# Kernel optimization log

Hardware: AMD Instinct MI355X
Metric: run time of the kernel (lower is better)

Reference implementation:

```python
import jax, jax.numpy as jnp
import numpy as np

B, D, H, O = 16384, 256, 64, 256


def setup_inputs() -> dict:
    key = jax.random.key(0)
    ks = jax.random.split(key, 7)
    s1 = 1.0  # Linear(1,H): fan_in=1 -> U(-1,1)
    sH = 1.0 / np.sqrt(H)
    sD = 1.0 / np.sqrt(D)
    return {
        "x": jax.random.normal(ks[0], (B, D), dtype=jnp.float32),
        "W1": jax.random.uniform(ks[1], (D, H), jnp.float32, -s1, s1),
        "b1": jax.random.uniform(ks[2], (D, H), jnp.float32, -s1, s1),
        "W2": jax.random.uniform(ks[3], (D, H), jnp.float32, -sH, sH),
        "b2": jax.random.uniform(ks[4], (D,), jnp.float32, -sH, sH),
        "Wc": jax.random.uniform(ks[5], (O, D), jnp.float32, -sD, sD),
        "bc": jax.random.uniform(ks[6], (O,), jnp.float32, -sD, sD),
    }


def reference(x, W1, b1, W2, b2, Wc, bc):
    # Per-feature tiny MLP, batched over the feature axis D.
    # hidden: [B, D, H]
    h = jax.nn.relu(x[:, :, None] * W1[None, :, :] + b1[None, :, :])
    # collapse hidden -> scalar per feature: [B, D]
    u = jnp.einsum("bdh,dh->bd", h, W2) + b2[None, :]
    # combiner Linear(D, O)
    return u @ Wc.T + bc[None, :]
```

## Files before the change

kernel.cpp:

```cpp
#include <hip/hip_runtime.h>
#include <hip/hip_fp16.h>

#define B_N 16384
#define D_N 256
#define H_N 64
#define O_N 256

typedef unsigned int u32;
typedef unsigned short u16;
typedef _Float16 f16;
typedef __attribute__((ext_vector_type(2))) _Float16 f16x2;
typedef __attribute__((ext_vector_type(8))) _Float16 f16x8;
typedef __attribute__((ext_vector_type(4))) float f32x4;
typedef __attribute__((ext_vector_type(4))) u32 uint4v;
typedef __attribute__((ext_vector_type(4))) u16 u16x4;

__device__ u32 g_Wp [D_N * 32];
__device__ u32 g_Bp [D_N * 32];
__device__ u32 g_W2p[D_N * 32];
__device__ __attribute__((aligned(16))) u16 g_Wch[O_N * D_N];
__device__ __attribute__((aligned(16))) u16 g_Uf[B_N * D_N];

union HU { f16 h; u16 b; };

static __device__ __forceinline__ u32 packh2(float a, float b) {
  f16x2 p = {(f16)a, (f16)b};
  return __builtin_bit_cast(u32, p);
}
static __device__ __forceinline__ u16 f16b(float a) { HU u; u.h = (f16)a; return u.b; }
static __device__ __forceinline__ f16x2 ash2(u32 w) { return __builtin_bit_cast(f16x2, w); }

#if __has_builtin(__builtin_amdgcn_fdot2)
#define FDOT2(a, b, c) __builtin_amdgcn_fdot2((a), (b), (c), false)
#else
#define FDOT2(a, b, c) \
  fmaf((float)(a)[0], (float)(b)[0], fmaf((float)(a)[1], (float)(b)[1], (c)))
#endif

__global__ __launch_bounds__(256) void prep(
    const float* __restrict__ W1, const float* __restrict__ b1,
    const float* __restrict__ W2, const float* __restrict__ Wc) {
  const int t = blockIdx.x * 256 + threadIdx.x;
  if ((t & 1) == 0) {
    const int d = t >> 6, j = (t & 63) >> 1;
    const int idx = d * 32 + j;
    g_Wp[idx]  = packh2(W1[t], W1[t + 1]);
    g_Bp[idx]  = packh2(b1[t], b1[t + 1]);
    g_W2p[idx] = packh2(W2[t], W2[t + 1]);
  }
  const int i4 = t * 4;
  const f32x4 v = *reinterpret_cast<const f32x4*>(Wc + i4);
  u16x4 s;
#pragma unroll
  for (int q = 0; q < 4; ++q) s[q] = f16b(v[q]);
  *reinterpret_cast<u16x4*>(g_Wch + i4) = s;
}

__global__ __launch_bounds__(256) void kan_p1(const float* __restrict__ x,
                                              const float* __restrict__ b2) {
  const int tid = threadIdx.x;
  const int b   = (blockIdx.x >> 4) * 256 + tid;
  const int d0  = (blockIdx.x & 15) * 16;

  f32x4 xr[4];
#pragma unroll
  for (int c = 0; c < 4; ++c)
    xr[c] = *reinterpret_cast<const f32x4*>(x + b * D_N + d0 + c * 4);

  float uo[16];
#pragma unroll
  for (int c = 0; c < 4; ++c) {
#pragma unroll
    for (int e = 0; e < 4; ++e) {
      const int dd = c * 4 + e;
      const int d  = d0 + dd;
      const f16 hx = (f16)xr[c][e];
      const f16x2 xx = {hx, hx};
      float acc = 0.f;
      const u32* __restrict__ wp  = g_Wp  + d * 32;
      const u32* __restrict__ bp  = g_Bp  + d * 32;
      const u32* __restrict__ w2p = g_W2p + d * 32;
#pragma unroll
      for (int j = 0; j < 32; ++j) {
        f16x2 tv = __builtin_elementwise_fma(xx, ash2(wp[j]), ash2(bp[j]));
        tv = __builtin_elementwise_max(tv, (f16x2){(f16)0.f, (f16)0.f});
        acc = FDOT2(tv, ash2(w2p[j]), acc);
      }
      uo[dd] = acc + b2[d];
    }
  }

  const int base = ((b >> 4) * 32 + (d0 >> 3)) * 128 + (b & 15) * 8;
#pragma unroll
  for (int half = 0; half < 2; ++half) {
    union { u16 h[8]; uint4v v; } pk;
#pragma unroll
    for (int e = 0; e < 8; ++e) pk.h[e] = f16b(uo[half * 8 + e]);
    *reinterpret_cast<uint4v*>(g_Uf + base + half * 128) = pk.v;
  }
}

__global__ __launch_bounds__(256) void kan_p2(const float* __restrict__ bc,
                                              float* __restrict__ out) {
  const int t    = threadIdx.x;
  const int wv   = t >> 6, dl = t & 63;
  const int mt   = blockIdx.x;
  const int n0   = wv * 64;
  const int mrow = dl & 15;
  const int kgrp = dl >> 4;
  const int b0   = mt * 16;

  f32x4 acc2[4];
#pragma unroll
  for (int j = 0; j < 4; ++j) acc2[j] = (f32x4)(0.f);

#pragma unroll
  for (int ks = 0; ks < 8; ++ks) {
    const int k0 = ks * 32 + kgrp * 8;
    const f16x8 afrag = *reinterpret_cast<const f16x8*>(
        g_Uf + (mt * 32 + ks * 4 + kgrp) * 128 + mrow * 8);
#pragma unroll
    for (int j = 0; j < 4; ++j) {
      const f16x8 bfrag = *reinterpret_cast<const f16x8*>(
          g_Wch + (n0 + j * 16 + mrow) * D_N + k0);
      acc2[j] = __builtin_amdgcn_mfma_f32_16x16x32_f16(afrag, bfrag, acc2[j],
                                                       0, 0, 0);
    }
  }

#pragma unroll
  for (int j = 0; j < 4; ++j) {
    const int colg = n0 + j * 16 + mrow;
    const float bcv = bc[colg];
#pragma unroll
    for (int q = 0; q < 4; ++q) {
      const int rowg = b0 + kgrp * 4 + q;
      out[rowg * O_N + colg] = acc2[j][q] + bcv;
    }
  }
}

extern "C" void kernel_launch(void* const* d_in, const int* in_sizes, int n_in,
                              void* d_out, int out_size, void* d_ws, size_t ws_size,
                              hipStream_t stream) {
  const float* x  = (const float*)d_in[0];
  const float* W1 = (const float*)d_in[1];
  const float* b1 = (const float*)d_in[2];
  const float* W2 = (const float*)d_in[3];
  const float* b2 = (const float*)d_in[4];
  const float* Wc = (const float*)d_in[5];
  const float* bc = (const float*)d_in[6];
  float* out = (float*)d_out;

  prep<<<dim3(D_N * H_N / 256), dim3(256), 0, stream>>>(W1, b1, W2, Wc);
  kan_p1<<<dim3((B_N / 256) * (D_N / 16)), dim3(256), 0, stream>>>(x, b2);
  kan_p2<<<dim3(B_N / 16), dim3(256), 0, stream>>>(bc, out);
}
```

Baseline: 118.4 us.

## Stage per-feature weights in LDS via async DMA and reuse across rows

The three packed fp16 weight arrays are interleaved into one buffer, and each wave copies its 8 features' weights into LDS with global_load_lds. In the old code every thread read weights from global memory through scalar loads. Each thread now handles 4 batch rows for 8 features, so every LDS weight vector read is reused across 4 rows. Blocks cover 32 features with a launch bound of 2 waves per SIMD. The tradeoff is higher register pressure from 32 packed x values and a raw vmcnt wait.

```diff
diff --git a/kernel.cpp b/kernel.cpp
--- a/kernel.cpp
+++ b/kernel.cpp
@@ -15,9 +15,7 @@
 typedef __attribute__((ext_vector_type(4))) u32 uint4v;
 typedef __attribute__((ext_vector_type(4))) u16 u16x4;
 
-__device__ u32 g_Wp [D_N * 32];
-__device__ u32 g_Bp [D_N * 32];
-__device__ u32 g_W2p[D_N * 32];
+__device__ __attribute__((aligned(16))) u32 g_Wf[D_N * 96];
 __device__ __attribute__((aligned(16))) u16 g_Wch[O_N * D_N];
 __device__ __attribute__((aligned(16))) u16 g_Uf[B_N * D_N];
 
@@ -37,16 +35,21 @@
   fmaf((float)(a)[0], (float)(b)[0], fmaf((float)(a)[1], (float)(b)[1], (c)))
 #endif
 
+static __device__ __forceinline__ void dma16(const u32* g, u32* l) {
+  __builtin_amdgcn_global_load_lds(
+      (const __attribute__((address_space(1))) u32*)g,
+      (__attribute__((address_space(3))) u32*)l, 16, 0, 0);
+}
+
 __global__ __launch_bounds__(256) void prep(
     const float* __restrict__ W1, const float* __restrict__ b1,
     const float* __restrict__ W2, const float* __restrict__ Wc) {
   const int t = blockIdx.x * 256 + threadIdx.x;
   if ((t & 1) == 0) {
     const int d = t >> 6, j = (t & 63) >> 1;
-    const int idx = d * 32 + j;
-    g_Wp[idx]  = packh2(W1[t], W1[t + 1]);
-    g_Bp[idx]  = packh2(b1[t], b1[t + 1]);
-    g_W2p[idx] = packh2(W2[t], W2[t + 1]);
+    g_Wf[d * 96 + j]      = packh2(W1[t], W1[t + 1]);
+    g_Wf[d * 96 + 32 + j] = packh2(b1[t], b1[t + 1]);
+    g_Wf[d * 96 + 64 + j] = packh2(W2[t], W2[t + 1]);
   }
   const int i4 = t * 4;
   const f32x4 v = *reinterpret_cast<const f32x4*>(Wc + i4);
@@ -56,47 +59,76 @@
   *reinterpret_cast<u16x4*>(g_Wch + i4) = s;
 }
 
-__global__ __launch_bounds__(256) void kan_p1(const float* __restrict__ x,
-                                              const float* __restrict__ b2) {
-  const int tid = threadIdx.x;
-  const int b   = (blockIdx.x >> 4) * 256 + tid;
-  const int d0  = (blockIdx.x & 15) * 16;
+__global__ __launch_bounds__(256, 2) void kan_p1(const float* __restrict__ x,
+                                                 const float* __restrict__ b2) {
+  __shared__ u32 wlds[4 * 768];
 
-  f32x4 xr[4];
+  const int tid  = threadIdx.x;
+  const int lane = tid & 63;
+  const int wv   = tid >> 6;
+  const int bs   = blockIdx.x >> 3;
+  const int dg   = blockIdx.x & 7;
+  const int d0   = dg * 32 + wv * 8;
+  const int rb   = bs * 256 + lane;
+
+  {
+    const u32* src = g_Wf + d0 * 96;
+    u32* dst = wlds + wv * 768;
 #pragma unroll
-  for (int c = 0; c < 4; ++c)
-    xr[c] = *reinterpret_cast<const f32x4*>(x + b * D_N + d0 + c * 4);
+    for (int i = 0; i < 3; ++i) dma16(src + i * 256 + lane * 4, dst + i * 256);
+  }
 
-  float uo[16];
+  f16x2 xx[4][8];
 #pragma unroll
-  for (int c = 0; c < 4; ++c) {
+  for (int r = 0; r < 4; ++r) {
+    const float* xp = x + (size_t)(rb + r * 64) * D_N + d0;
+    const f32x4 a = *reinterpret_cast<const f32x4*>(xp);
+    const f32x4 b = *reinterpret_cast<const f32x4*>(xp + 4);
 #pragma unroll
     for (int e = 0; e < 4; ++e) {
-      const int dd = c * 4 + e;
-      const int d  = d0 + dd;
-      const f16 hx = (f16)xr[c][e];
-      const f16x2 xx = {hx, hx};
-      float acc = 0.f;
-      const u32* __restrict__ wp  = g_Wp  + d * 32;
-      const u32* __restrict__ bp  = g_Bp  + d * 32;
-      const u32* __restrict__ w2p = g_W2p + d * 32;
-#pragma unroll
-      for (int j = 0; j < 32; ++j) {
-        f16x2 tv = __builtin_elementwise_fma(xx, ash2(wp[j]), ash2(bp[j]));
-        tv = __builtin_elementwise_max(tv, (f16x2){(f16)0.f, (f16)0.f});
-        acc = FDOT2(tv, ash2(w2p[j]), acc);
-      }
-      uo[dd] = acc + b2[d];
+      const f16 ha = (f16)a[e], hb = (f16)b[e];
+      xx[r][e]     = (f16x2){ha, ha};
+      xx[r][4 + e] = (f16x2){hb, hb};
     }
   }
 
-  const int base = ((b >> 4) * 32 + (d0 >> 3)) * 128 + (b & 15) * 8;
+  asm volatile("s_waitcnt vmcnt(0)" ::: "memory");
+
+  const u32* wl = wlds + wv * 768;
+  uint4v pkv[4];
 #pragma unroll
-  for (int half = 0; half < 2; ++half) {
-    union { u16 h[8]; uint4v v; } pk;
+  for (int dd = 0; dd < 8; ++dd) {
+    const float b2v = b2[d0 + dd];
+    float acc[4] = {0.f, 0.f, 0.f, 0.f};
 #pragma unroll
-    for (int e = 0; e < 8; ++e) pk.h[e] = f16b(uo[half * 8 + e]);
-    *reinterpret_cast<uint4v*>(g_Uf + base + half * 128) = pk.v;
+    for (int jq = 0; jq < 8; ++jq) {
+      const uint4v w1q = *reinterpret_cast<const uint4v*>(wl + dd * 96 + jq * 4);
+      const uint4v b1q = *reinterpret_cast<const uint4v*>(wl + dd * 96 + 32 + jq * 4);
+      const uint4v w2q = *reinterpret_cast<const uint4v*>(wl + dd * 96 + 64 + jq * 4);
+#pragma unroll
+      for (int k = 0; k < 4; ++k) {
+        const f16x2 w1 = ash2(w1q[k]), bb = ash2(b1q[k]), w2 = ash2(w2q[k]);
+#pragma unroll
+        for (int r = 0; r < 4; ++r) {
+          f16x2 tv = __builtin_elementwise_fma(xx[r][dd], w1, bb);
+          tv = __builtin_elementwise_max(tv, (f16x2){(f16)0.f, (f16)0.f});
+          acc[r] = FDOT2(tv, w2, acc[r]);
+        }
+      }
+    }
+#pragma unroll
+    for (int r = 0; r < 4; ++r) {
+      const u16 hv = f16b(acc[r] + b2v);
+      if ((dd & 1) == 0) pkv[r][dd >> 1] = (u32)hv;
+      else               pkv[r][dd >> 1] |= ((u32)hv) << 16;
+    }
+  }
+
+#pragma unroll
+  for (int r = 0; r < 4; ++r) {
+    const int row = rb + r * 64;
+    u16* p = g_Uf + (size_t)((row >> 4) * 32 + (d0 >> 3)) * 128 + (row & 15) * 8;
+    *reinterpret_cast<uint4v*>(p) = pkv[r];
   }
 }
 
@@ -153,6 +185,6 @@
   float* out = (float*)d_out;
 
   prep<<<dim3(D_N * H_N / 256), dim3(256), 0, stream>>>(W1, b1, W2, Wc);
-  kan_p1<<<dim3((B_N / 256) * (D_N / 16)), dim3(256), 0, stream>>>(x, b2);
+  kan_p1<<<dim3((B_N / 256) * (D_N / 32)), dim3(256), 0, stream>>>(x, b2);
   kan_p2<<<dim3(B_N / 16), dim3(256), 0, stream>>>(bc, out);
 }
```

Result: slower. 125.6 us (+6.0%).
